# Optimization experiments

Hardware: AMD Instinct MI355X
Metric: run time of the kernel (lower is better)

The kernel has to match this reference:

```python
import jax, jax.numpy as jnp
import numpy as np

BS, MA, H, NH = 64, 64, 64, 4  # molecules, max atoms per molecule, hsize, n_heads


def _lengths():
    # deterministic ragged molecule sizes in [24, 64]
    return np.array([24 + (7 * i) % 41 for i in range(BS)], dtype=np.int64)


def _scopes():
    lengths = _lengths()
    N = int(lengths.sum())  # 2774
    scope = np.zeros((BS, MA), dtype=np.int64)      # pad slots gather row 0 (zeros)
    rev = np.zeros((N,), dtype=np.int64)            # flat atom -> b*MA + slot
    pos = 1                                          # flat row 0 is the zero pad row
    for b, L in enumerate(lengths):
        scope[b, :L] = np.arange(pos, pos + L)
        rev[pos - 1:pos - 1 + L] = b * MA + np.arange(L)
        pos += L
    return scope, rev, N


def setup_inputs() -> dict:
    key = jax.random.key(0)
    k0, k1, k2, k3 = jax.random.split(key, 4)
    scope, rev, N = _scopes()
    inputs = jax.random.normal(k0, (N + 1, H), dtype=jnp.float32)
    inputs = inputs.at[0].set(0.0)  # zero pad row, as in graphretro flat tensors
    Wa_pair = jax.random.normal(k1, (H, H * NH), dtype=jnp.float32) * (1.0 / np.sqrt(H))
    Wa_score = jax.random.normal(k2, (H, NH), dtype=jnp.float32) * (1.0 / np.sqrt(H))
    W_proj = jax.random.normal(k3, (H * NH, H), dtype=jnp.float32) * (1.0 / np.sqrt(H * NH))
    return {
        "inputs": inputs,
        "scope_tensor": jnp.asarray(scope),
        "scope_rev_tensor": jnp.asarray(rev),
        "Wa_pair": Wa_pair,
        "Wa_score": Wa_score,
        "W_proj": W_proj,
    }


def reference(inputs, scope_tensor, scope_rev_tensor, Wa_pair, Wa_score, W_proj):
    bs, ma = scope_tensor.shape
    h = inputs.shape[1]
    nh = Wa_score.shape[1]
    # flat_to_batch: [bs, ma, h]; pad slots pull the zero row 0
    c_batch = inputs[scope_tensor]
    # get_pair: pairwise sum of atom embeddings -> [bs, ma, ma, h]
    atom_pair = c_batch[:, :, None, :] + c_batch[:, None, :, :]
    # Wa_pair (no bias) + relu, viewed as [bs, ma, ma, h, nh]
    total_att = jax.nn.relu(atom_pair @ Wa_pair).reshape(bs, ma, ma, h, nh)
    # einsum '...hn,hjn->...jn' with j==1, then sigmoid -> [bs, ma, ma, nh]
    att_score = jax.nn.sigmoid(jnp.einsum('bijhn,hn->bijn', total_att, Wa_score))
    # att_score * c_atom[b,j,h], summed over j -> [bs, ma, h, nh]
    c_sum = jnp.einsum('bijn,bjh->bihn', att_score, c_batch)
    # view to [bs, ma, h*nh] (h-major, matching torch .view) and project
    c_atom_att = c_sum.reshape(bs, ma, h * nh) @ W_proj  # [bs, ma, h]
    c_mol_att = c_atom_att.sum(axis=1)  # [bs, h]
    # batch_to_flat + prepend zero row -> [N+1, h]
    flat = c_atom_att.reshape(bs * ma, h)[scope_rev_tensor]
    c_atom_att_flat = jnp.concatenate([jnp.zeros((1, h), flat.dtype), flat], axis=0)
    return (c_mol_att, c_atom_att_flat)
```

## Files before the change

kernel.cpp:

```cpp
#include <hip/hip_runtime.h>
#include <stdint.h>

typedef _Float16 h2 __attribute__((ext_vector_type(2)));
typedef _Float16 h8 __attribute__((ext_vector_type(8)));
typedef float f32x4 __attribute__((ext_vector_type(4)));
typedef unsigned int u32;
typedef unsigned short u16;

#define CB_STR 72
#define WA_STR 68
#define WP_STR 68
#define P_STR  68
#define CW_STR 68
#define AB_STR 72

__device__ __forceinline__ u32 pk2(float a, float b) {
    return __builtin_bit_cast(u32, __builtin_amdgcn_cvt_pkrtz(a, b));
}
__device__ __forceinline__ h8 frag4(u32 a, u32 b, u32 c, u32 d) {
    return __builtin_bit_cast(h8, make_uint4(a, b, c, d));
}

__global__ __launch_bounds__(512, 1) void atom_attn(
    const float* __restrict__ inputs,
    const int*   __restrict__ scope,
    const float* __restrict__ Wa_pair,
    const float* __restrict__ Wa_score,
    const float* __restrict__ W_proj,
    float* __restrict__ out_mol,
    float* __restrict__ out_flat)
{
    __shared__ __align__(16) u16 s_cb[64 * CB_STR];
    __shared__ __align__(16) u16 s_wa[64 * WA_STR];
    __shared__ __align__(16) u16 s_wp[64 * WP_STR];
    __shared__ __align__(16) u16 s_p [64 * P_STR ];
    __shared__ __align__(16) u16 s_cw[64 * CW_STR];
    __shared__ __align__(16) u16 s_ab[64 * AB_STR];
    __shared__ __align__(16) u32 s_ws[32];

    const int t = threadIdx.x;
    const int w = t >> 6, l = t & 63;
    const int ml = l & 15, q = l >> 4;
    const int n = blockIdx.x;
    const int b = blockIdx.y;

    if (t < 256) {
        const int jp = (t & 31) * 2;
        const int pp = t >> 5;
        const int r0 = scope[b * 64 + jp];
        const int r1 = scope[b * 64 + jp + 1];
        const f32x4 a0 = *(const f32x4*)(inputs + (size_t)r0 * 64 + pp * 8);
        const f32x4 a1 = *(const f32x4*)(inputs + (size_t)r0 * 64 + pp * 8 + 4);
        const f32x4 b0 = *(const f32x4*)(inputs + (size_t)r1 * 64 + pp * 8);
        const f32x4 b1 = *(const f32x4*)(inputs + (size_t)r1 * 64 + pp * 8 + 4);
        *(uint4*)&s_cb[jp * CB_STR + pp * 8] =
            make_uint4(pk2(a0[0], a0[1]), pk2(a0[2], a0[3]), pk2(a1[0], a1[1]), pk2(a1[2], a1[3]));
        *(uint4*)&s_cb[(jp + 1) * CB_STR + pp * 8] =
            make_uint4(pk2(b0[0], b0[1]), pk2(b0[2], b0[3]), pk2(b1[0], b1[1]), pk2(b1[2], b1[3]));
    }
    {
        float a[8];
        #pragma unroll
        for (int e = 0; e < 8; ++e)
            a[e] = Wa_pair[(w * 8 + e) * 256 + 4 * l + n];
        *(uint4*)&s_wa[l * WA_STR + w * 8] =
            make_uint4(pk2(a[0], a[1]), pk2(a[2], a[3]), pk2(a[4], a[5]), pk2(a[6], a[7]));
    }
    {
        u32 v[4];
        #pragma unroll
        for (int e = 0; e < 4; ++e) {
            const int hh = w * 4 + e;
            const float v0 = W_proj[(8 * hh + n) * 64 + l];
            const float v1 = W_proj[(8 * hh + 4 + n) * 64 + l];
            v[e] = pk2(v0, v1);
        }
        *(uint4*)&s_wp[l * WP_STR + w * 8] = make_uint4(v[0], v[1], v[2], v[3]);
    }
    if (t < 32) {
        s_ws[t] = pk2(Wa_score[(2 * t) * 4 + n], Wa_score[(2 * t + 1) * 4 + n]);
    }
    __syncthreads();

    if (w < 4) {
        f32x4 D[4];
        #pragma unroll
        for (int jt = 0; jt < 4; ++jt) D[jt] = (f32x4)0.f;
        #pragma unroll
        for (int ks = 0; ks < 2; ++ks) {
            const uint2 x0 = *(const uint2*)&s_wa[(w * 16 + ml) * WA_STR + ks * 32 + q * 8];
            const uint2 x1 = *(const uint2*)&s_wa[(w * 16 + ml) * WA_STR + ks * 32 + q * 8 + 4];
            const h8 af = frag4(x0.x, x0.y, x1.x, x1.y);
            #pragma unroll
            for (int jt = 0; jt < 4; ++jt) {
                const h8 bf = __builtin_bit_cast(h8,
                    *(const uint4*)&s_cb[(jt * 16 + ml) * CB_STR + ks * 32 + q * 8]);
                D[jt] = __builtin_amdgcn_mfma_f32_16x16x32_f16(af, bf, D[jt], 0, 0, 0);
            }
        }
        #pragma unroll
        for (int jt = 0; jt < 4; ++jt) {
            const int j = jt * 16 + ml;
            *(uint2*)&s_p[j * P_STR + w * 16 + q * 4] =
                make_uint2(pk2(D[jt][0], D[jt][1]), pk2(D[jt][2], D[jt][3]));
        }
    } else {
        const int w4 = w - 4;
        f32x4 D[4];
        #pragma unroll
        for (int ot = 0; ot < 4; ++ot) D[ot] = (f32x4)0.f;
        #pragma unroll
        for (int ks = 0; ks < 2; ++ks) {
            const h8 af = __builtin_bit_cast(h8,
                *(const uint4*)&s_cb[(w4 * 16 + ml) * CB_STR + ks * 32 + q * 8]);
            #pragma unroll
            for (int ot = 0; ot < 4; ++ot) {
                const uint2 y0 = *(const uint2*)&s_wp[(ot * 16 + ml) * WP_STR + ks * 32 + q * 8];
                const uint2 y1 = *(const uint2*)&s_wp[(ot * 16 + ml) * WP_STR + ks * 32 + q * 8 + 4];
                const h8 bf = frag4(y0.x, y0.y, y1.x, y1.y);
                D[ot] = __builtin_amdgcn_mfma_f32_16x16x32_f16(af, bf, D[ot], 0, 0, 0);
            }
        }
        #pragma unroll
        for (int ot = 0; ot < 4; ++ot) {
            const int o = ot * 16 + ml;
            *(uint2*)&s_cw[o * CW_STR + w4 * 16 + q * 4] =
                make_uint2(pk2(D[ot][0], D[ot][1]), pk2(D[ot][2], D[ot][3]));
        }
    }
    __syncthreads();

    {
        u32 pj_u[32];
        #pragma unroll
        for (int k = 0; k < 16; ++k) {
            const uint2 vv = *(const uint2*)&s_p[l * P_STR + k * 4];
            pj_u[2 * k] = vv.x; pj_u[2 * k + 1] = vv.y;
        }
        u32 ws_u[32];
        #pragma unroll
        for (int k = 0; k < 8; ++k) {
            const uint4 vv = *(const uint4*)&s_ws[k * 4];
            ws_u[4 * k] = vv.x; ws_u[4 * k + 1] = vv.y;
            ws_u[4 * k + 2] = vv.z; ws_u[4 * k + 3] = vv.w;
        }
        const h2 zero2 = {(_Float16)0.f, (_Float16)0.f};
        #pragma unroll
        for (int ii = 0; ii < 8; ++ii) {
            const int i = w * 8 + ii;
            const u16* pir = &s_p[i * P_STR];
            float s0 = 0.f, s1 = 0.f;
            #pragma unroll
            for (int c8 = 0; c8 < 8; ++c8) {
                const uint2 u0 = *(const uint2*)&pir[c8 * 8];
                const uint2 u1 = *(const uint2*)&pir[c8 * 8 + 4];
                const u32 pe[4] = {u0.x, u0.y, u1.x, u1.y};
                #pragma unroll
                for (int e = 0; e < 4; ++e) {
                    const h2 pi2 = __builtin_bit_cast(h2, pe[e]);
                    const h2 pj2 = __builtin_bit_cast(h2, pj_u[c8 * 4 + e]);
                    h2 tv = pi2 + pj2;
                    tv = __builtin_elementwise_max(tv, zero2);
                    if (e & 1)
                        s1 = __builtin_amdgcn_fdot2(tv,
                                __builtin_bit_cast(h2, ws_u[c8 * 4 + e]), s1, false);
                    else
                        s0 = __builtin_amdgcn_fdot2(tv,
                                __builtin_bit_cast(h2, ws_u[c8 * 4 + e]), s0, false);
                }
            }
            const float s = s0 + s1;
            const float a = 1.f / (1.f + __expf(-s));
            const _Float16 ah = (_Float16)a;
            s_ab[i * AB_STR + l] = __builtin_bit_cast(u16, ah);
        }
    }
    __syncthreads();

    {
        const int mt = w & 3, nh2 = w >> 2;
        h8 af3[2];
        #pragma unroll
        for (int ks = 0; ks < 2; ++ks)
            af3[ks] = __builtin_bit_cast(h8,
                *(const uint4*)&s_ab[(mt * 16 + ml) * AB_STR + ks * 32 + q * 8]);
        #pragma unroll
        for (int nx = 0; nx < 2; ++nx) {
            const int nt = nh2 * 2 + nx;
            f32x4 D = (f32x4)0.f;
            #pragma unroll
            for (int ks = 0; ks < 2; ++ks) {
                const uint2 y0 = *(const uint2*)&s_cw[(nt * 16 + ml) * CW_STR + ks * 32 + q * 8];
                const uint2 y1 = *(const uint2*)&s_cw[(nt * 16 + ml) * CW_STR + ks * 32 + q * 8 + 4];
                const h8 bf = frag4(y0.x, y0.y, y1.x, y1.y);
                D = __builtin_amdgcn_mfma_f32_16x16x32_f16(af3[ks], bf, D, 0, 0, 0);
            }
            const int o = nt * 16 + ml;
            float colsum = 0.f;
            #pragma unroll
            for (int r = 0; r < 4; ++r) {
                const int i = mt * 16 + q * 4 + r;
                const int row = scope[b * 64 + i];
                if (row > 0) atomicAdd(out_flat + (size_t)row * 64 + o, D[r]);
                colsum += D[r];
            }
            colsum += __shfl_xor(colsum, 16, 64);
            colsum += __shfl_xor(colsum, 32, 64);
            if (q == 0) atomicAdd(out_mol + b * 64 + o, colsum);
        }
    }
}

extern "C" void kernel_launch(void* const* d_in, const int* in_sizes, int n_in,
                              void* d_out, int out_size, void* d_ws, size_t ws_size,
                              hipStream_t stream) {
    const float* inputs   = (const float*)d_in[0];
    const int*   scope    = (const int*)d_in[1];
    const float* Wa_pair  = (const float*)d_in[3];
    const float* Wa_score = (const float*)d_in[4];
    const float* W_proj   = (const float*)d_in[5];
    float* out = (float*)d_out;

    (void)hipMemsetAsync(d_out, 0, (size_t)out_size, stream);

    dim3 grid(4, 64);
    atom_attn<<<grid, 512, 0, stream>>>(inputs, scope, Wa_pair, Wa_score,
                                        W_proj, out, out + 64 * 64);
}
```

Measured before the change: 75.02 us.

## Process all heads per block, drop memset and atomics with direct stores

The grid changes from one block per (head, molecule) to one block per molecule, and each block now handles all four heads. The final projection reduces over all heads inside the block, so outputs are written with plain stores instead of atomics. The hipMemsetAsync is removed and only the zero pad row is cleared. The cost is a heavier per-block workload: the score loop becomes 32 rows per wave, and only 64 blocks run on a device with many more compute units, so parallelism drops.

```diff
diff --git a/kernel.cpp b/kernel.cpp
--- a/kernel.cpp
+++ b/kernel.cpp
@@ -7,12 +7,12 @@
 typedef unsigned int u32;
 typedef unsigned short u16;
 
-#define CB_STR 72
-#define WA_STR 68
-#define WP_STR 68
-#define P_STR  68
-#define CW_STR 68
-#define AB_STR 72
+#define CB_STR  72
+#define WA_STR  68
+#define WP_STR  68
+#define P_STR   68
+#define CW_STR  68
+#define ABF_STR 264
 
 __device__ __forceinline__ u32 pk2(float a, float b) {
     return __builtin_bit_cast(u32, __builtin_amdgcn_cvt_pkrtz(a, b));
@@ -20,6 +20,11 @@
 __device__ __forceinline__ h8 frag4(u32 a, u32 b, u32 c, u32 d) {
     return __builtin_bit_cast(h8, make_uint4(a, b, c, d));
 }
+
+union SMemU {
+    struct { u16 wa[4][64 * WA_STR]; u16 wp[4][64 * WP_STR]; } p1;
+    u16 ab[64 * ABF_STR];
+};
 
 __global__ __launch_bounds__(512, 1) void atom_attn(
     const float* __restrict__ inputs,
@@ -30,20 +35,51 @@
     float* __restrict__ out_mol,
     float* __restrict__ out_flat)
 {
+    __shared__ __align__(16) SMemU s_u;
     __shared__ __align__(16) u16 s_cb[64 * CB_STR];
-    __shared__ __align__(16) u16 s_wa[64 * WA_STR];
-    __shared__ __align__(16) u16 s_wp[64 * WP_STR];
-    __shared__ __align__(16) u16 s_p [64 * P_STR ];
-    __shared__ __align__(16) u16 s_cw[64 * CW_STR];
-    __shared__ __align__(16) u16 s_ab[64 * AB_STR];
-    __shared__ __align__(16) u32 s_ws[32];
+    __shared__ __align__(16) u16 s_p [4][64 * P_STR];
+    __shared__ __align__(16) u16 s_cw[4][64 * CW_STR];
+    __shared__ __align__(16) u32 s_ws[4 * 32];
+    __shared__ __align__(16) float s_msum[8][16];
 
     const int t = threadIdx.x;
     const int w = t >> 6, l = t & 63;
     const int ml = l & 15, q = l >> 4;
-    const int n = blockIdx.x;
-    const int b = blockIdx.y;
-
+    const int b = blockIdx.x;
+
+    {
+        const int hp = t >> 4;
+        const int cc = (t & 15) * 16;
+        const float* r0p = Wa_pair + (2 * hp) * 256 + cc;
+        const float* r1p = Wa_pair + (2 * hp + 1) * 256 + cc;
+        #pragma unroll
+        for (int v = 0; v < 4; ++v) {
+            const f32x4 x0 = *(const f32x4*)(r0p + v * 4);
+            const f32x4 x1 = *(const f32x4*)(r1p + v * 4);
+            #pragma unroll
+            for (int e = 0; e < 4; ++e) {
+                const int c = cc + v * 4 + e;
+                const int n = c & 3, ho = c >> 2;
+                *(u32*)&s_u.p1.wa[n][ho * WA_STR + 2 * hp] = pk2(x0[e], x1[e]);
+            }
+        }
+    }
+    {
+        const int n = t >> 7, r = t & 127;
+        const int hh = r >> 2, o0 = (r & 3) * 16;
+        const float* c0p = W_proj + (8 * hh + n) * 64 + o0;
+        const float* c1p = W_proj + (8 * hh + 4 + n) * 64 + o0;
+        #pragma unroll
+        for (int v = 0; v < 4; ++v) {
+            const f32x4 x0 = *(const f32x4*)(c0p + v * 4);
+            const f32x4 x1 = *(const f32x4*)(c1p + v * 4);
+            #pragma unroll
+            for (int e = 0; e < 4; ++e) {
+                const int o = o0 + v * 4 + e;
+                *(u32*)&s_u.p1.wp[n][o * WP_STR + 2 * hh] = pk2(x0[e], x1[e]);
+            }
+        }
+    }
     if (t < 256) {
         const int jp = (t & 31) * 2;
         const int pp = t >> 5;
@@ -58,97 +94,100 @@
         *(uint4*)&s_cb[(jp + 1) * CB_STR + pp * 8] =
             make_uint4(pk2(b0[0], b0[1]), pk2(b0[2], b0[3]), pk2(b1[0], b1[1]), pk2(b1[2], b1[3]));
     }
-    {
-        float a[8];
-        #pragma unroll
-        for (int e = 0; e < 8; ++e)
-            a[e] = Wa_pair[(w * 8 + e) * 256 + 4 * l + n];
-        *(uint4*)&s_wa[l * WA_STR + w * 8] =
-            make_uint4(pk2(a[0], a[1]), pk2(a[2], a[3]), pk2(a[4], a[5]), pk2(a[6], a[7]));
-    }
-    {
-        u32 v[4];
-        #pragma unroll
-        for (int e = 0; e < 4; ++e) {
-            const int hh = w * 4 + e;
-            const float v0 = W_proj[(8 * hh + n) * 64 + l];
-            const float v1 = W_proj[(8 * hh + 4 + n) * 64 + l];
-            v[e] = pk2(v0, v1);
-        }
-        *(uint4*)&s_wp[l * WP_STR + w * 8] = make_uint4(v[0], v[1], v[2], v[3]);
-    }
-    if (t < 32) {
-        s_ws[t] = pk2(Wa_score[(2 * t) * 4 + n], Wa_score[(2 * t + 1) * 4 + n]);
-    }
+    if (t < 128) {
+        const int n = t >> 5, hh = t & 31;
+        s_ws[n * 32 + hh] = pk2(Wa_score[(2 * hh) * 4 + n], Wa_score[(2 * hh + 1) * 4 + n]);
+    }
+    if (b == 0 && t < 64) out_flat[t] = 0.f;
     __syncthreads();
 
     if (w < 4) {
-        f32x4 D[4];
-        #pragma unroll
-        for (int jt = 0; jt < 4; ++jt) D[jt] = (f32x4)0.f;
+        const int n = w;
+        f32x4 D[4][4];
+        #pragma unroll
+        for (int mt = 0; mt < 4; ++mt)
+            #pragma unroll
+            for (int jt = 0; jt < 4; ++jt) D[mt][jt] = (f32x4)0.f;
         #pragma unroll
         for (int ks = 0; ks < 2; ++ks) {
-            const uint2 x0 = *(const uint2*)&s_wa[(w * 16 + ml) * WA_STR + ks * 32 + q * 8];
-            const uint2 x1 = *(const uint2*)&s_wa[(w * 16 + ml) * WA_STR + ks * 32 + q * 8 + 4];
-            const h8 af = frag4(x0.x, x0.y, x1.x, x1.y);
+            h8 bfj[4];
+            #pragma unroll
+            for (int jt = 0; jt < 4; ++jt)
+                bfj[jt] = __builtin_bit_cast(h8,
+                    *(const uint4*)&s_cb[(jt * 16 + ml) * CB_STR + ks * 32 + q * 8]);
+            #pragma unroll
+            for (int mt = 0; mt < 4; ++mt) {
+                const uint2 x0 = *(const uint2*)&s_u.p1.wa[n][(mt * 16 + ml) * WA_STR + ks * 32 + q * 8];
+                const uint2 x1 = *(const uint2*)&s_u.p1.wa[n][(mt * 16 + ml) * WA_STR + ks * 32 + q * 8 + 4];
+                const h8 af = frag4(x0.x, x0.y, x1.x, x1.y);
+                #pragma unroll
+                for (int jt = 0; jt < 4; ++jt)
+                    D[mt][jt] = __builtin_amdgcn_mfma_f32_16x16x32_f16(af, bfj[jt], D[mt][jt], 0, 0, 0);
+            }
+        }
+        #pragma unroll
+        for (int mt = 0; mt < 4; ++mt)
             #pragma unroll
             for (int jt = 0; jt < 4; ++jt) {
-                const h8 bf = __builtin_bit_cast(h8,
-                    *(const uint4*)&s_cb[(jt * 16 + ml) * CB_STR + ks * 32 + q * 8]);
-                D[jt] = __builtin_amdgcn_mfma_f32_16x16x32_f16(af, bf, D[jt], 0, 0, 0);
-            }
-        }
-        #pragma unroll
-        for (int jt = 0; jt < 4; ++jt) {
-            const int j = jt * 16 + ml;
-            *(uint2*)&s_p[j * P_STR + w * 16 + q * 4] =
-                make_uint2(pk2(D[jt][0], D[jt][1]), pk2(D[jt][2], D[jt][3]));
-        }
+                const int j = jt * 16 + ml;
+                *(uint2*)&s_p[n][j * P_STR + mt * 16 + q * 4] =
+                    make_uint2(pk2(D[mt][jt][0], D[mt][jt][1]), pk2(D[mt][jt][2], D[mt][jt][3]));
+            }
     } else {
-        const int w4 = w - 4;
-        f32x4 D[4];
-        #pragma unroll
-        for (int ot = 0; ot < 4; ++ot) D[ot] = (f32x4)0.f;
+        const int n = w - 4;
+        f32x4 D[4][4];
+        #pragma unroll
+        for (int mt = 0; mt < 4; ++mt)
+            #pragma unroll
+            for (int ot = 0; ot < 4; ++ot) D[mt][ot] = (f32x4)0.f;
         #pragma unroll
         for (int ks = 0; ks < 2; ++ks) {
-            const h8 af = __builtin_bit_cast(h8,
-                *(const uint4*)&s_cb[(w4 * 16 + ml) * CB_STR + ks * 32 + q * 8]);
+            h8 afm[4];
+            #pragma unroll
+            for (int mt = 0; mt < 4; ++mt)
+                afm[mt] = __builtin_bit_cast(h8,
+                    *(const uint4*)&s_cb[(mt * 16 + ml) * CB_STR + ks * 32 + q * 8]);
             #pragma unroll
             for (int ot = 0; ot < 4; ++ot) {
-                const uint2 y0 = *(const uint2*)&s_wp[(ot * 16 + ml) * WP_STR + ks * 32 + q * 8];
-                const uint2 y1 = *(const uint2*)&s_wp[(ot * 16 + ml) * WP_STR + ks * 32 + q * 8 + 4];
+                const uint2 y0 = *(const uint2*)&s_u.p1.wp[n][(ot * 16 + ml) * WP_STR + ks * 32 + q * 8];
+                const uint2 y1 = *(const uint2*)&s_u.p1.wp[n][(ot * 16 + ml) * WP_STR + ks * 32 + q * 8 + 4];
                 const h8 bf = frag4(y0.x, y0.y, y1.x, y1.y);
-                D[ot] = __builtin_amdgcn_mfma_f32_16x16x32_f16(af, bf, D[ot], 0, 0, 0);
-            }
-        }
-        #pragma unroll
-        for (int ot = 0; ot < 4; ++ot) {
-            const int o = ot * 16 + ml;
-            *(uint2*)&s_cw[o * CW_STR + w4 * 16 + q * 4] =
-                make_uint2(pk2(D[ot][0], D[ot][1]), pk2(D[ot][2], D[ot][3]));
-        }
-    }
-    __syncthreads();
-
-    {
+                #pragma unroll
+                for (int mt = 0; mt < 4; ++mt)
+                    D[mt][ot] = __builtin_amdgcn_mfma_f32_16x16x32_f16(afm[mt], bf, D[mt][ot], 0, 0, 0);
+            }
+        }
+        #pragma unroll
+        for (int mt = 0; mt < 4; ++mt)
+            #pragma unroll
+            for (int ot = 0; ot < 4; ++ot) {
+                const int o = ot * 16 + ml;
+                *(uint2*)&s_cw[n][o * CW_STR + mt * 16 + q * 4] =
+                    make_uint2(pk2(D[mt][ot][0], D[mt][ot][1]), pk2(D[mt][ot][2], D[mt][ot][3]));
+            }
+    }
+    __syncthreads();
+
+    {
+        const int n = w & 3, ih = w >> 2;
         u32 pj_u[32];
         #pragma unroll
         for (int k = 0; k < 16; ++k) {
-            const uint2 vv = *(const uint2*)&s_p[l * P_STR + k * 4];
+            const uint2 vv = *(const uint2*)&s_p[n][l * P_STR + k * 4];
             pj_u[2 * k] = vv.x; pj_u[2 * k + 1] = vv.y;
         }
         u32 ws_u[32];
         #pragma unroll
         for (int k = 0; k < 8; ++k) {
-            const uint4 vv = *(const uint4*)&s_ws[k * 4];
+            const uint4 vv = *(const uint4*)&s_ws[n * 32 + k * 4];
             ws_u[4 * k] = vv.x; ws_u[4 * k + 1] = vv.y;
             ws_u[4 * k + 2] = vv.z; ws_u[4 * k + 3] = vv.w;
         }
         const h2 zero2 = {(_Float16)0.f, (_Float16)0.f};
-        #pragma unroll
-        for (int ii = 0; ii < 8; ++ii) {
-            const int i = w * 8 + ii;
-            const u16* pir = &s_p[i * P_STR];
+        #pragma unroll 4
+        for (int ii = 0; ii < 32; ++ii) {
+            const int i = ih * 32 + ii;
+            const u16* pir = &s_p[n][i * P_STR];
             float s0 = 0.f, s1 = 0.f;
             #pragma unroll
             for (int c8 = 0; c8 < 8; ++c8) {
@@ -172,43 +211,47 @@
             const float s = s0 + s1;
             const float a = 1.f / (1.f + __expf(-s));
             const _Float16 ah = (_Float16)a;
-            s_ab[i * AB_STR + l] = __builtin_bit_cast(u16, ah);
-        }
-    }
-    __syncthreads();
-
-    {
-        const int mt = w & 3, nh2 = w >> 2;
-        h8 af3[2];
-        #pragma unroll
-        for (int ks = 0; ks < 2; ++ks)
-            af3[ks] = __builtin_bit_cast(h8,
-                *(const uint4*)&s_ab[(mt * 16 + ml) * AB_STR + ks * 32 + q * 8]);
-        #pragma unroll
-        for (int nx = 0; nx < 2; ++nx) {
-            const int nt = nh2 * 2 + nx;
-            f32x4 D = (f32x4)0.f;
-            #pragma unroll
-            for (int ks = 0; ks < 2; ++ks) {
-                const uint2 y0 = *(const uint2*)&s_cw[(nt * 16 + ml) * CW_STR + ks * 32 + q * 8];
-                const uint2 y1 = *(const uint2*)&s_cw[(nt * 16 + ml) * CW_STR + ks * 32 + q * 8 + 4];
-                const h8 bf = frag4(y0.x, y0.y, y1.x, y1.y);
-                D = __builtin_amdgcn_mfma_f32_16x16x32_f16(af3[ks], bf, D, 0, 0, 0);
-            }
-            const int o = nt * 16 + ml;
-            float colsum = 0.f;
+            s_u.ab[i * ABF_STR + n * 64 + l] = __builtin_bit_cast(u16, ah);
+        }
+    }
+    __syncthreads();
+
+    {
+        const int nt = w >> 1, mh = w & 1;
+        f32x4 D3[2];
+        D3[0] = (f32x4)0.f; D3[1] = (f32x4)0.f;
+        #pragma unroll
+        for (int ks = 0; ks < 8; ++ks) {
+            const int n = ks >> 1;
+            const uint2 y0 = *(const uint2*)&s_cw[n][(nt * 16 + ml) * CW_STR + (ks & 1) * 32 + q * 8];
+            const uint2 y1 = *(const uint2*)&s_cw[n][(nt * 16 + ml) * CW_STR + (ks & 1) * 32 + q * 8 + 4];
+            const h8 bf = frag4(y0.x, y0.y, y1.x, y1.y);
+            #pragma unroll
+            for (int mtl = 0; mtl < 2; ++mtl) {
+                const int mt = mh * 2 + mtl;
+                const h8 af = __builtin_bit_cast(h8,
+                    *(const uint4*)&s_u.ab[(mt * 16 + ml) * ABF_STR + ks * 32 + q * 8]);
+                D3[mtl] = __builtin_amdgcn_mfma_f32_16x16x32_f16(af, bf, D3[mtl], 0, 0, 0);
+            }
+        }
+        const int o = nt * 16 + ml;
+        float colsum = 0.f;
+        #pragma unroll
+        for (int mtl = 0; mtl < 2; ++mtl)
             #pragma unroll
             for (int r = 0; r < 4; ++r) {
-                const int i = mt * 16 + q * 4 + r;
+                const int i = (mh * 2 + mtl) * 16 + q * 4 + r;
                 const int row = scope[b * 64 + i];
-                if (row > 0) atomicAdd(out_flat + (size_t)row * 64 + o, D[r]);
-                colsum += D[r];
-            }
-            colsum += __shfl_xor(colsum, 16, 64);
-            colsum += __shfl_xor(colsum, 32, 64);
-            if (q == 0) atomicAdd(out_mol + b * 64 + o, colsum);
-        }
-    }
+                if (row > 0) out_flat[(size_t)row * 64 + o] = D3[mtl][r];
+                colsum += D3[mtl][r];
+            }
+        colsum += __shfl_xor(colsum, 16, 64);
+        colsum += __shfl_xor(colsum, 32, 64);
+        if (l < 16) s_msum[w][ml] = colsum;
+    }
+    __syncthreads();
+    if (t < 64)
+        out_mol[b * 64 + t] = s_msum[2 * (t >> 4)][t & 15] + s_msum[2 * (t >> 4) + 1][t & 15];
 }
 
 extern "C" void kernel_launch(void* const* d_in, const int* in_sizes, int n_in,
@@ -221,9 +264,7 @@
     const float* W_proj   = (const float*)d_in[5];
     float* out = (float*)d_out;
 
-    (void)hipMemsetAsync(d_out, 0, (size_t)out_size, stream);
-
-    dim3 grid(4, 64);
+    dim3 grid(64);
     atom_attn<<<grid, 512, 0, stream>>>(inputs, scope, Wa_pair, Wa_score,
                                         W_proj, out, out + 64 * 64);
 }
```

Result: slower. 84.89 us (+13.2%).
